# Kernel optimization log

Hardware: AMD Instinct MI355X
Metric: run time of the kernel (lower is better)

The kernel has to match this reference:

```python
import math
import jax, jax.numpy as jnp
import numpy as np

B, L, D, H = 4, 2048, 512, 8
DK = D // H  # d_keys = d_values = 64
KFAC = 3


def setup_inputs() -> dict:
    key = jax.random.key(0)
    ks = jax.random.split(key, 10)
    u_part = min(KFAC * int(math.ceil(math.log(L))), L)  # 24
    scale = 1.0 / math.sqrt(D)
    return {
        "queries": jax.random.normal(ks[0], (B, L, D), jnp.float32),
        "keys": jax.random.normal(ks[1], (B, L, D), jnp.float32),
        "values": jax.random.normal(ks[2], (B, L, D), jnp.float32),
        "index_sample": jax.random.randint(ks[3], (L, u_part), 0, L, jnp.int32),
        "Wq": jax.random.normal(ks[4], (D, D), jnp.float32) * scale,
        "bq": jnp.zeros((D,), jnp.float32),
        "Wk": jax.random.normal(ks[5], (D, D), jnp.float32) * scale,
        "bk": jnp.zeros((D,), jnp.float32),
        "Wv": jax.random.normal(ks[6], (D, D), jnp.float32) * scale,
        "bv": jnp.zeros((D,), jnp.float32),
        "Wo": jax.random.normal(ks[7], (D, D), jnp.float32) * scale,
        "bo": jnp.zeros((D,), jnp.float32),
    }


def reference(queries, keys, values, index_sample, Wq, bq, Wk, bk, Wv, bv, Wo, bo):
    b, q_len, d_out = queries.shape
    k_len = keys.shape[1]
    # projections -> [B, H, L, DK]
    q = (queries @ Wq + bq).reshape(b, q_len, H, DK).transpose(0, 2, 1, 3)
    k = (keys @ Wk + bk).reshape(b, k_len, H, DK).transpose(0, 2, 1, 3)
    v = (values @ Wv + bv).reshape(b, k_len, H, DK).transpose(0, 2, 1, 3)

    n_top = min(KFAC * int(math.ceil(math.log(q_len))), q_len)  # u

    # --- _prob_qk: sampled QK scores to pick sparse queries ---
    # k_sample: [B, H, q_len, sample_k, DK]
    k_sample = k[:, :, index_sample, :]
    q_k_sample = jnp.einsum("bhld,bhlsd->bhls", q, k_sample)
    m = jnp.max(q_k_sample, axis=-1) - jnp.sum(q_k_sample, axis=-1) / k_len
    _, m_top = jax.lax.top_k(m, n_top)  # [B, H, u]

    q_reduce = jnp.take_along_axis(q, m_top[..., None], axis=2)  # [B, H, u, DK]
    scores_top = jnp.einsum("bhud,bhkd->bhuk", q_reduce, k) / math.sqrt(d_out)

    # --- masked (causal) branch: mask_flag=True ---
    causal = jnp.triu(jnp.ones((q_len, k_len), bool), 1)
    indicator = causal[m_top]  # [B, H, u, k_len]
    scores_top = jnp.where(indicator, -jnp.inf, scores_top)

    attn = jax.nn.softmax(scores_top, axis=-1)  # [B, H, u, k_len]
    context = jnp.cumsum(v, axis=2)  # default context for non-selected queries
    attn_values = jnp.einsum("bhuk,bhkd->bhud", attn, v)

    bidx = jnp.arange(b)[:, None, None]
    hidx = jnp.arange(H)[None, :, None]
    context = context.at[bidx, hidx, m_top].set(attn_values)

    # mix=False: transpose back to [B, L, H, DV] then merge heads
    context = context.transpose(0, 2, 1, 3).reshape(b, q_len, H * DK)
    out = context @ Wo + bo  # dropout_rate=0 / inference: identity
    return out
```

## Files before the change

kernel.cpp:

```cpp
#include <hip/hip_runtime.h>
#include <hip/hip_bf16.h>
#include <math.h>

#define Bq 4
#define Lq 2048
#define Dq 512
#define Hq 8
#define DKq 64
#define Uq 24
#define TSCAN 16
#define NTILE (Lq / TSCAN)
#define NSUP 16
#define JCH 256
#define NCH (Lq / JCH)
#define TKCH 8

typedef unsigned short ushort_t;
typedef unsigned long long u64;
typedef __attribute__((ext_vector_type(8))) short bfrag8;
typedef __attribute__((ext_vector_type(4))) float facc4;

__device__ inline ushort_t bf16_rne(float f) {
  unsigned u = __float_as_uint(f);
  u += 0x7FFF + ((u >> 16) & 1);
  return (ushort_t)(u >> 16);
}
__device__ inline float bf16f(ushort_t h) {
  return __uint_as_float(((unsigned)h) << 16);
}
__device__ inline unsigned fkey(float f) {
  unsigned u = __float_as_uint(f);
  return (u & 0x80000000u) ? ~u : (u | 0x80000000u);
}
__device__ __forceinline__ void gl2lds16(const void* g, void* l) {
  __builtin_amdgcn_global_load_lds(
      (const __attribute__((address_space(1))) unsigned*)g,
      (__attribute__((address_space(3))) unsigned*)l, 16, 0, 0);
}

__global__ __launch_bounds__(256) void cast_all(
    const float* __restrict__ xq, const float* __restrict__ xk,
    const float* __restrict__ xv, ushort_t* __restrict__ qh,
    ushort_t* __restrict__ ql, ushort_t* __restrict__ kh,
    ushort_t* __restrict__ kl, ushort_t* __restrict__ vh) {
  int z = blockIdx.y;
  const float* x = z == 0 ? xq : (z == 1 ? xk : xv);
  ushort_t* hi = z == 0 ? qh : (z == 1 ? kh : vh);
  ushort_t* lo = z == 0 ? ql : kl;
  int t = blockIdx.x * 256 + threadIdx.x;
  float4 v = *(const float4*)&x[(size_t)t * 4];
  ushort_t h0 = bf16_rne(v.x), h1 = bf16_rne(v.y), h2 = bf16_rne(v.z),
           h3 = bf16_rne(v.w);
  ushort4 hh = {h0, h1, h2, h3};
  *(ushort4*)&hi[(size_t)t * 4] = hh;
  if (z < 2) {
    ushort4 ll = {bf16_rne(v.x - bf16f(h0)), bf16_rne(v.y - bf16f(h1)),
                  bf16_rne(v.z - bf16f(h2)), bf16_rne(v.w - bf16f(h3))};
    *(ushort4*)&lo[(size_t)t * 4] = ll;
  }
}

__global__ __launch_bounds__(256) void transpose_cast4(
    const float* __restrict__ W0, const float* __restrict__ W1,
    const float* __restrict__ W2, const float* __restrict__ W3,
    ushort_t* __restrict__ T0h, ushort_t* __restrict__ T0l,
    ushort_t* __restrict__ T1h, ushort_t* __restrict__ T1l,
    ushort_t* __restrict__ T2h, ushort_t* __restrict__ T3h) {
  __shared__ float tile[32][33];
  int z = blockIdx.z;
  const float* W = z == 0 ? W0 : (z == 1 ? W1 : (z == 2 ? W2 : W3));
  ushort_t* Th = z == 0 ? T0h : (z == 1 ? T1h : (z == 2 ? T2h : T3h));
  ushort_t* Tl = z == 0 ? T0l : (z == 1 ? T1l : nullptr);
  int k0 = blockIdx.x * 32, n0 = blockIdx.y * 32;
  int tx = threadIdx.x & 31, ty = threadIdx.x >> 5;
  for (int r = ty; r < 32; r += 8)
    tile[tx][r] = W[(size_t)(k0 + r) * 512 + n0 + tx];
  __syncthreads();
  for (int r = ty; r < 32; r += 8) {
    float v = tile[r][tx];
    ushort_t h = bf16_rne(v);
    Th[(size_t)(n0 + r) * 512 + k0 + tx] = h;
    if (Tl) Tl[(size_t)(n0 + r) * 512 + k0 + tx] = bf16_rne(v - bf16f(h));
  }
}

__global__ __launch_bounds__(256) void gemm_qkv(
    const ushort_t* __restrict__ Aqh, const ushort_t* __restrict__ Aql,
    const ushort_t* __restrict__ Akh, const ushort_t* __restrict__ Akl,
    const ushort_t* __restrict__ Avh,
    const ushort_t* __restrict__ Wqh, const ushort_t* __restrict__ Wql,
    const ushort_t* __restrict__ Wkh, const ushort_t* __restrict__ Wkl,
    const ushort_t* __restrict__ Wvh,
    const float* __restrict__ bq, const float* __restrict__ bk,
    const float* __restrict__ bv,
    float* __restrict__ qo, float* __restrict__ ko, float* __restrict__ vo) {
  __shared__ ushort_t Ash[128][32], Asl[128][32];
  __shared__ ushort_t Bsh[128][32], Bsl[128][32];
  int which = blockIdx.z;
  const ushort_t* Ah = which == 0 ? Aqh : (which == 1 ? Akh : Avh);
  const ushort_t* Al = which == 0 ? Aql : Akl;
  const ushort_t* Bh = which == 0 ? Wqh : (which == 1 ? Wkh : Wvh);
  const ushort_t* Bl = which == 0 ? Wql : Wkl;
  const float* bias = which == 0 ? bq : (which == 1 ? bk : bv);
  float* C = which == 0 ? qo : (which == 1 ? ko : vo);
  const bool split = which < 2;

  int bm = blockIdx.x, bn = blockIdx.y;
  int tid = threadIdx.x;
  int wave = tid >> 6, lane = tid & 63;
  int wm = (wave & 1) * 64, wn = (wave >> 1) * 64;
  int quad = lane >> 4, lm = lane & 15;
  int srow = tid >> 2;
  int slc = (((tid & 3) ^ ((tid >> 3) & 3))) * 8;
  int sphys = (tid & 3) * 8;
  int rsw = (quad ^ ((lm >> 1) & 3)) * 8;
  facc4 acc[4][4] = {};

  for (int k0 = 0; k0 < 512; k0 += 32) {
#pragma unroll
    for (int p = 0; p < 2; ++p) {
      int row = srow + p * 64;
      size_t ga = (size_t)(bm * 128 + row) * 512 + k0 + slc;
      size_t gb = (size_t)(bn * 128 + row) * 512 + k0 + slc;
      gl2lds16(&Ah[ga], &Ash[row][sphys]);
      gl2lds16(&Bh[gb], &Bsh[row][sphys]);
      if (split) {
        gl2lds16(&Al[ga], &Asl[row][sphys]);
        gl2lds16(&Bl[gb], &Bsl[row][sphys]);
      }
    }
    __syncthreads();
    bfrag8 afh[4], afl[4], bfh[4], bfl[4];
#pragma unroll
    for (int mt = 0; mt < 4; ++mt) {
      afh[mt] = *(bfrag8*)&Ash[wm + mt * 16 + lm][rsw];
      if (split) afl[mt] = *(bfrag8*)&Asl[wm + mt * 16 + lm][rsw];
    }
#pragma unroll
    for (int nt = 0; nt < 4; ++nt) {
      bfh[nt] = *(bfrag8*)&Bsh[wn + nt * 16 + lm][rsw];
      if (split) bfl[nt] = *(bfrag8*)&Bsl[wn + nt * 16 + lm][rsw];
    }
#pragma unroll
    for (int mt = 0; mt < 4; ++mt)
#pragma unroll
      for (int nt = 0; nt < 4; ++nt) {
        facc4 a = acc[mt][nt];
        a = __builtin_amdgcn_mfma_f32_16x16x32_bf16(afh[mt], bfh[nt], a, 0, 0, 0);
        if (split) {
          a = __builtin_amdgcn_mfma_f32_16x16x32_bf16(afl[mt], bfh[nt], a, 0, 0, 0);
          a = __builtin_amdgcn_mfma_f32_16x16x32_bf16(afh[mt], bfl[nt], a, 0, 0, 0);
        }
        acc[mt][nt] = a;
      }
    __syncthreads();
  }
#pragma unroll
  for (int mt = 0; mt < 4; ++mt)
#pragma unroll
    for (int nt = 0; nt < 4; ++nt) {
      int col = bn * 128 + wn + nt * 16 + lm;
      float bv2 = bias[col];
#pragma unroll
      for (int r = 0; r < 4; ++r) {
        int row = bm * 128 + wm + mt * 16 + quad * 4 + r;
        C[(size_t)row * 512 + col] = acc[mt][nt][r] + bv2;
      }
    }
}

__global__ __launch_bounds__(256) void gemm_bf16(
    const ushort_t* __restrict__ A, const ushort_t* __restrict__ Bt,
    const float* __restrict__ bias, float* __restrict__ C) {
  __shared__ ushort_t As[128][32];
  __shared__ ushort_t Bs[128][32];
  int bm = blockIdx.x, bn = blockIdx.y;
  int tid = threadIdx.x;
  int wave = tid >> 6, lane = tid & 63;
  int wm = (wave & 1) * 64, wn = (wave >> 1) * 64;
  int quad = lane >> 4, lm = lane & 15;
  int srow = tid >> 2;
  int slc = (((tid & 3) ^ ((tid >> 3) & 3))) * 8;
  int sphys = (tid & 3) * 8;
  int rsw = (quad ^ ((lm >> 1) & 3)) * 8;
  facc4 acc[4][4] = {};

  for (int k0 = 0; k0 < 512; k0 += 32) {
#pragma unroll
    for (int p = 0; p < 2; ++p) {
      int row = srow + p * 64;
      gl2lds16(&A[(size_t)(bm * 128 + row) * 512 + k0 + slc], &As[row][sphys]);
      gl2lds16(&Bt[(size_t)(bn * 128 + row) * 512 + k0 + slc], &Bs[row][sphys]);
    }
    __syncthreads();
    bfrag8 af[4], bf[4];
#pragma unroll
    for (int mt = 0; mt < 4; ++mt)
      af[mt] = *(bfrag8*)&As[wm + mt * 16 + lm][rsw];
#pragma unroll
    for (int nt = 0; nt < 4; ++nt)
      bf[nt] = *(bfrag8*)&Bs[wn + nt * 16 + lm][rsw];
#pragma unroll
    for (int mt = 0; mt < 4; ++mt)
#pragma unroll
      for (int nt = 0; nt < 4; ++nt)
        acc[mt][nt] = __builtin_amdgcn_mfma_f32_16x16x32_bf16(
            af[mt], bf[nt], acc[mt][nt], 0, 0, 0);
    __syncthreads();
  }
#pragma unroll
  for (int mt = 0; mt < 4; ++mt)
#pragma unroll
    for (int nt = 0; nt < 4; ++nt) {
      int col = bn * 128 + wn + nt * 16 + lm;
      float bv = bias[col];
#pragma unroll
      for (int r = 0; r < 4; ++r) {
        int row = bm * 128 + wm + mt * 16 + quad * 4 + r;
        C[(size_t)row * 512 + col] = acc[mt][nt][r] + bv;
      }
    }
}

__global__ __launch_bounds__(256) void compute_m(
    const float* __restrict__ q, const float* __restrict__ k,
    const int* __restrict__ idxs, float* __restrict__ m) {
  int wave = threadIdx.x >> 6, lane = threadIdx.x & 63;
  int lq = lane >> 4, dq = lane & 15;
  int slot = (blockIdx.x * 4 + wave) * 4 + lq;
  int l = slot & (Lq - 1);
  int bh = slot >> 11;
  int h = bh & (Hq - 1), b = bh >> 3;
  float4 qv = *(const float4*)&q[((size_t)b * Lq + l) * Dq + h * DKq + dq * 4];
  const float* kb = &k[(size_t)b * Lq * Dq + h * DKq + dq * 4];
  const int* ib = &idxs[l * Uq];
  float mx = -INFINITY, sm = 0.f;
#pragma unroll
  for (int s = 0; s < Uq; ++s) {
    int j = ib[s];
    float4 kv = *(const float4*)&kb[(size_t)j * Dq];
    float p = qv.x * kv.x + qv.y * kv.y + qv.z * kv.z + qv.w * kv.w;
    p += __shfl_xor(p, 1, 64);
    p += __shfl_xor(p, 2, 64);
    p += __shfl_xor(p, 4, 64);
    p += __shfl_xor(p, 8, 64);
    mx = fmaxf(mx, p);
    sm += p;
  }
  if (dq == 0) m[slot] = mx - sm * (1.0f / Lq);
}

__device__ inline void bitonic256_desc(u64* s, int tid) {
  for (int k = 2; k <= 256; k <<= 1) {
    for (int j = k >> 1; j > 0; j >>= 1) {
      int p = tid ^ j;
      u64 mine = s[tid], other = s[p];
      u64 mx = mine > other ? mine : other;
      u64 mn = mine > other ? other : mine;
      bool dir = (tid & k) == 0;
      bool lower = tid < p;
      u64 res = dir ? (lower ? mx : mn) : (lower ? mn : mx);
      __syncthreads();
      s[tid] = res;
      __syncthreads();
    }
  }
}

__global__ __launch_bounds__(256) void topk_stage1(
    const float* __restrict__ m, u64* __restrict__ cand) {
  __shared__ u64 s[256];
  int bh = blockIdx.x >> 3;
  int ch = blockIdx.x & 7;
  int tid = threadIdx.x;
  int gidx = ch * 256 + tid;
  float v = m[(size_t)bh * Lq + gidx];
  s[tid] = ((u64)fkey(v) << 32) | (u64)(Lq - 1 - gidx);
  __syncthreads();
  bitonic256_desc(s, tid);
  if (tid < Uq) cand[((size_t)bh * TKCH + ch) * Uq + tid] = s[tid];
}

__global__ __launch_bounds__(256) void topk_stage2(
    const u64* __restrict__ cand, int* __restrict__ mtop,
    int* __restrict__ repl) {
  __shared__ u64 s[256];
  __shared__ int mt[Uq];
  int bh = blockIdx.x;
  int tid = threadIdx.x;
  s[tid] = (tid < TKCH * Uq) ? cand[(size_t)bh * TKCH * Uq + tid] : 0ull;
  __syncthreads();
  bitonic256_desc(s, tid);
  if (tid < Uq) {
    int idx = Lq - 1 - (int)(s[tid] & 0xFFFFFFFFull);
    mtop[bh * Uq + tid] = idx;
    mt[tid] = idx;
  }
  __syncthreads();
  for (int l = tid; l < Lq; l += 256) {
    int u = -1;
#pragma unroll
    for (int t = 0; t < Uq; ++t)
      if (mt[t] == l) u = t;
    repl[(size_t)bh * Lq + l] = u;
  }
}

#define JT 256
#define JS 64

__global__ __launch_bounds__(256) void scores_kernel(
    const float* __restrict__ q, const float* __restrict__ k,
    const int* __restrict__ mtop, float* __restrict__ scg) {
  __shared__ float qs[Uq][DKq + 1];
  __shared__ float ks[JS][DKq + 1];
  __shared__ int i0s[Uq];
  int bh = blockIdx.y;
  int jt = blockIdx.x;
  int h = bh & (Hq - 1);
  int b = bh >> 3;
  int tid = threadIdx.x;
  if (tid < Uq) i0s[tid] = mtop[bh * Uq + tid];
  __syncthreads();
  for (int s = tid; s < Uq * 16; s += 256) {
    int u = s >> 4, qd = (s & 15) * 4;
    float4 t = *(const float4*)&q[((size_t)b * Lq + i0s[u]) * Dq + h * DKq + qd];
    qs[u][qd] = t.x; qs[u][qd + 1] = t.y; qs[u][qd + 2] = t.z; qs[u][qd + 3] = t.w;
  }
  int jp = tid & 31;
  int ug = tid >> 5;
  const float scale = 0.044194173824159216f;
  for (int sub = 0; sub < JT / JS; ++sub) {
    int jbase = jt * JT + sub * JS;
    __syncthreads();
    for (int s = tid; s < JS * 16; s += 256) {
      int j = s >> 4, qd = (s & 15) * 4;
      float4 t = *(const float4*)&k[((size_t)b * Lq + jbase + j) * Dq + h * DKq + qd];
      ks[j][qd] = t.x; ks[j][qd + 1] = t.y; ks[j][qd + 2] = t.z; ks[j][qd + 3] = t.w;
    }
    __syncthreads();
    float acc[3][2] = {};
    int j0 = jp * 2, j1 = j0 + 1;
#pragma unroll 8
    for (int d = 0; d < DKq; ++d) {
      float k0 = ks[j0][d], k1 = ks[j1][d];
#pragma unroll
      for (int uu = 0; uu < 3; ++uu) {
        float qv = qs[ug * 3 + uu][d];
        acc[uu][0] += qv * k0;
        acc[uu][1] += qv * k1;
      }
    }
#pragma unroll
    for (int uu = 0; uu < 3; ++uu) {
      int u = ug * 3 + uu;
      scg[((size_t)(bh * Uq + u)) * Lq + jbase + j0] = acc[uu][0] * scale;
      scg[((size_t)(bh * Uq + u)) * Lq + jbase + j1] = acc[uu][1] * scale;
    }
  }
}

__global__ __launch_bounds__(256) void softmax_pv_partial(
    const float* __restrict__ scg, const float* __restrict__ v,
    const int* __restrict__ mtop, float* __restrict__ pmax,
    float* __restrict__ psum, float* __restrict__ pvp) {
  int blk = blockIdx.y;
  int jc = blockIdx.x;
  int bh = blk / Uq;
  int h = bh & (Hq - 1);
  int b = bh >> 3;
  int n = mtop[blk] + 1;
  int j0 = jc * JCH;
  if (j0 >= n) return;
  int cnt = min(JCH, n - j0);
  int tid = threadIdx.x, wave = tid >> 6, lane = tid & 63;
  __shared__ float es[JCH];
  __shared__ float red[4][DKq];
  __shared__ float rr[4];

  const float* row = &scg[(size_t)blk * Lq + j0];
  float mx = (tid < cnt) ? row[tid] : -INFINITY;
#pragma unroll
  for (int off = 32; off; off >>= 1) mx = fmaxf(mx, __shfl_xor(mx, off, 64));
  if (lane == 0) rr[wave] = mx;
  __syncthreads();
  mx = fmaxf(fmaxf(rr[0], rr[1]), fmaxf(rr[2], rr[3]));
  __syncthreads();

  float e = (tid < cnt) ? __expf(row[tid] - mx) : 0.f;
  es[tid] = e;
  float sm = e;
#pragma unroll
  for (int off = 32; off; off >>= 1) sm += __shfl_xor(sm, off, 64);
  if (lane == 0) rr[wave] = sm;
  __syncthreads();

  float acc = 0.f;
  const float* vb = &v[((size_t)b * Lq + j0) * Dq + h * DKq + lane];
  int jlo = wave * 64;
  int jhi = min(jlo + 64, cnt);
#pragma unroll 4
  for (int j = jlo; j < jhi; ++j) acc += es[j] * vb[(size_t)j * Dq];
  red[wave][lane] = acc;
  __syncthreads();
  if (wave == 0) {
    if (lane == 0) {
      pmax[blk * NCH + jc] = mx;
      psum[blk * NCH + jc] = rr[0] + rr[1] + rr[2] + rr[3];
    }
    pvp[((size_t)blk * NCH + jc) * DKq + lane] =
        red[0][lane] + red[1][lane] + red[2][lane] + red[3][lane];
  }
}

__global__ __launch_bounds__(128) void tile_sum(const float* __restrict__ v,
                                                float* __restrict__ tsum) {
  int blk = blockIdx.x;
  int tile = blk & (NTILE - 1);
  int b = blk >> 7;
  int d4 = threadIdx.x;
  float4 s = {0.f, 0.f, 0.f, 0.f};
  const float* base = &v[((size_t)b * Lq + tile * TSCAN) * Dq + d4 * 4];
#pragma unroll
  for (int r = 0; r < TSCAN; ++r) {
    float4 x = *(const float4*)&base[(size_t)r * Dq];
    s.x += x.x; s.y += x.y; s.z += x.z; s.w += x.w;
  }
  *(float4*)&tsum[((size_t)b * NTILE + tile) * Dq + d4 * 4] = s;
}

__global__ __launch_bounds__(128) void stile_sum(
    const float* __restrict__ tsum, float* __restrict__ stsum) {
  int blk = blockIdx.x;
  int s = blk & (NSUP - 1);
  int b = blk >> 4;
  int d4 = threadIdx.x;
  float4 acc = {0.f, 0.f, 0.f, 0.f};
  const float* tb = &tsum[((size_t)b * NTILE + s * 8) * Dq + d4 * 4];
#pragma unroll
  for (int i = 0; i < 8; ++i) {
    float4 t = *(const float4*)&tb[(size_t)i * Dq];
    acc.x += t.x; acc.y += t.y; acc.z += t.z; acc.w += t.w;
  }
  *(float4*)&stsum[((size_t)b * NSUP + s) * Dq + d4 * 4] = acc;
}

__global__ __launch_bounds__(128) void build_context(
    const float* __restrict__ v, const float* __restrict__ tsum,
    const float* __restrict__ stsum, const int* __restrict__ repl,
    const float* __restrict__ pmax, const float* __restrict__ psum,
    const float* __restrict__ pvp, ushort_t* __restrict__ ctxh) {
  int blk = blockIdx.x;
  int tile = blk & (NTILE - 1);
  int b = blk >> 7;
  int d4 = threadIdx.x;
  int h = d4 >> 4;
  int sup = tile >> 3;
  float4 run = {0.f, 0.f, 0.f, 0.f};
  const float* sb = &stsum[(size_t)b * NSUP * Dq + d4 * 4];
  for (int s = 0; s < sup; ++s) {
    float4 t = *(const float4*)&sb[(size_t)s * Dq];
    run.x += t.x; run.y += t.y; run.z += t.z; run.w += t.w;
  }
  const float* tb = &tsum[((size_t)b * NTILE + sup * 8) * Dq + d4 * 4];
  int rem = tile & 7;
  for (int i = 0; i < rem; ++i) {
    float4 t = *(const float4*)&tb[(size_t)i * Dq];
    run.x += t.x; run.y += t.y; run.z += t.z; run.w += t.w;
  }
  const int* replb = &repl[(size_t)(b * Hq + h) * Lq + tile * TSCAN];
  const float* vb = &v[((size_t)b * Lq + tile * TSCAN) * Dq + d4 * 4];
  ushort_t* cb = &ctxh[((size_t)b * Lq + tile * TSCAN) * Dq + d4 * 4];
#pragma unroll
  for (int r = 0; r < TSCAN; ++r) {
    float4 x = *(const float4*)&vb[(size_t)r * Dq];
    run.x += x.x; run.y += x.y; run.z += x.z; run.w += x.w;
    int u = replb[r];
    float4 val = run;
    if (u >= 0) {
      int l = tile * TSCAN + r;
      int blku = (b * Hq + h) * Uq + u;
      int nc = (l + JCH) / JCH;
      float gmax = -INFINITY;
      for (int c = 0; c < nc; ++c) gmax = fmaxf(gmax, pmax[blku * NCH + c]);
      float tot = 0.f;
      float4 acc = {0.f, 0.f, 0.f, 0.f};
      for (int c = 0; c < nc; ++c) {
        float wgt = __expf(pmax[blku * NCH + c] - gmax);
        tot += psum[blku * NCH + c] * wgt;
        float4 pv = *(const float4*)&pvp[((size_t)blku * NCH + c) * DKq +
                                         (d4 & 15) * 4];
        acc.x += pv.x * wgt; acc.y += pv.y * wgt;
        acc.z += pv.z * wgt; acc.w += pv.w * wgt;
      }
      float inv = 1.0f / tot;
      val.x = acc.x * inv; val.y = acc.y * inv;
      val.z = acc.z * inv; val.w = acc.w * inv;
    }
    ushort4 o = {bf16_rne(val.x), bf16_rne(val.y), bf16_rne(val.z),
                 bf16_rne(val.w)};
    *(ushort4*)&cb[(size_t)r * Dq] = o;
  }
}

extern "C" void kernel_launch(void* const* d_in, const int* in_sizes, int n_in,
                              void* d_out, int out_size, void* d_ws,
                              size_t ws_size, hipStream_t stream) {
  const float* queries = (const float*)d_in[0];
  const float* keys    = (const float*)d_in[1];
  const float* values  = (const float*)d_in[2];
  const int*   idxs    = (const int*)d_in[3];
  const float* Wq = (const float*)d_in[4];
  const float* bq = (const float*)d_in[5];
  const float* Wk = (const float*)d_in[6];
  const float* bk = (const float*)d_in[7];
  const float* Wv = (const float*)d_in[8];
  const float* bv = (const float*)d_in[9];
  const float* Wo = (const float*)d_in[10];
  const float* bo = (const float*)d_in[11];
  float* out = (float*)d_out;

  const size_t BLD = (size_t)Bq * Lq * Dq;
  char* w = (char*)d_ws;
  float* q    = (float*)w; w += BLD * 4;
  float* k    = (float*)w; w += BLD * 4;
  float* v    = (float*)w; w += BLD * 4;
  float* scg  = (float*)w; w += (size_t)Bq * Hq * Uq * Lq * 4;
  float* m    = (float*)w; w += (size_t)Bq * Hq * Lq * 4;
  float* tsum = (float*)w; w += (size_t)Bq * NTILE * Dq * 4;
  float* stsum= (float*)w; w += (size_t)Bq * NSUP * Dq * 4;
  int* mtop   = (int*)w;   w += Bq * Hq * Uq * 4;
  int* repl   = (int*)w;   w += (size_t)Bq * Hq * Lq * 4;
  float* pmax = (float*)w; w += (size_t)Bq * Hq * Uq * NCH * 4;
  float* psum = (float*)w; w += (size_t)Bq * Hq * Uq * NCH * 4;
  float* pvp  = (float*)w; w += (size_t)Bq * Hq * Uq * NCH * DKq * 4;
  u64* cand   = (u64*)w;   w += (size_t)Bq * Hq * TKCH * Uq * 8;
  ushort_t* ctxh = (ushort_t*)w; w += BLD * 2;
  ushort_t* Aqh = (ushort_t*)w; w += BLD * 2;
  ushort_t* Aql = (ushort_t*)w; w += BLD * 2;
  ushort_t* Akh = (ushort_t*)w; w += BLD * 2;
  ushort_t* Akl = (ushort_t*)w; w += BLD * 2;
  ushort_t* Avh = (ushort_t*)w; w += BLD * 2;
  const size_t WSZ = 512 * 512;
  ushort_t* Wqh = (ushort_t*)w; w += WSZ * 2;
  ushort_t* Wql = (ushort_t*)w; w += WSZ * 2;
  ushort_t* Wkh = (ushort_t*)w; w += WSZ * 2;
  ushort_t* Wkl = (ushort_t*)w; w += WSZ * 2;
  ushort_t* Wvh = (ushort_t*)w; w += WSZ * 2;
  ushort_t* Woh = (ushort_t*)w; w += WSZ * 2;

  {
    dim3 tgrid(16, 16, 4);
    transpose_cast4<<<tgrid, 256, 0, stream>>>(Wq, Wk, Wv, Wo, Wqh, Wql, Wkh,
                                               Wkl, Wvh, Woh);
  }

  {
    dim3 cgrid(BLD / 4 / 256, 3);
    cast_all<<<cgrid, 256, 0, stream>>>(queries, keys, values, Aqh, Aql, Akh,
                                        Akl, Avh);
  }

  {
    dim3 ggrid(64, 4, 3);
    gemm_qkv<<<ggrid, 256, 0, stream>>>(Aqh, Aql, Akh, Akl, Avh, Wqh, Wql,
                                        Wkh, Wkl, Wvh, bq, bk, bv, q, k, v);
  }

  compute_m<<<(Bq * Hq * Lq) / 16, 256, 0, stream>>>(q, k, idxs, m);
  topk_stage1<<<Bq * Hq * TKCH, 256, 0, stream>>>(m, cand);
  topk_stage2<<<Bq * Hq, 256, 0, stream>>>(cand, mtop, repl);

  {
    dim3 sgrid(Lq / JT, Bq * Hq);
    scores_kernel<<<sgrid, 256, 0, stream>>>(q, k, mtop, scg);
  }
  {
    dim3 pgrid(NCH, Bq * Hq * Uq);
    softmax_pv_partial<<<pgrid, 256, 0, stream>>>(scg, v, mtop, pmax, psum, pvp);
  }

  tile_sum<<<Bq * NTILE, 128, 0, stream>>>(v, tsum);
  stile_sum<<<Bq * NSUP, 128, 0, stream>>>(tsum, stsum);
  build_context<<<Bq * NTILE, 128, 0, stream>>>(v, tsum, stsum, repl, pmax,
                                                psum, pvp, ctxh);

  {
    dim3 ggrid(64, 4);
    gemm_bf16<<<ggrid, 256, 0, stream>>>(ctxh, Woh, bo, out);
  }
}
```

Baseline: 275.9 us.

## Merge prep kernels, fuse two-stage top-k, drop super-tile prefix kernel

Folds the weight transpose-cast into the activation cast kernel as one launch, with the extra grid row handling weights. Replaces the two bitonic-sort top-k kernels with a single per-head kernel that runs 24 rounds of register argmax plus a wave-shuffle reduction, and writes the replacement map directly. Removes the super-tile sum kernel, so build_context scans up to 127 tile sums serially. This saves three launches and the candidate buffer, at the cost of a longer serial prefix loop in build_context and a top-k that runs on only 32 blocks.

```diff
diff --git a/kernel.cpp b/kernel.cpp
--- a/kernel.cpp
+++ b/kernel.cpp
@@ -10,7 +10,6 @@
 #define Uq 24
 #define TSCAN 16
 #define NTILE (Lq / TSCAN)
-#define NSUP 16
 #define JCH 256
 #define NCH (Lq / JCH)
 #define TKCH 8
@@ -38,40 +37,42 @@
       (__attribute__((address_space(3))) unsigned*)l, 16, 0, 0);
 }
 
-__global__ __launch_bounds__(256) void cast_all(
+__global__ __launch_bounds__(256) void prep_all(
     const float* __restrict__ xq, const float* __restrict__ xk,
     const float* __restrict__ xv, ushort_t* __restrict__ qh,
     ushort_t* __restrict__ ql, ushort_t* __restrict__ kh,
-    ushort_t* __restrict__ kl, ushort_t* __restrict__ vh) {
-  int z = blockIdx.y;
-  const float* x = z == 0 ? xq : (z == 1 ? xk : xv);
-  ushort_t* hi = z == 0 ? qh : (z == 1 ? kh : vh);
-  ushort_t* lo = z == 0 ? ql : kl;
-  int t = blockIdx.x * 256 + threadIdx.x;
-  float4 v = *(const float4*)&x[(size_t)t * 4];
-  ushort_t h0 = bf16_rne(v.x), h1 = bf16_rne(v.y), h2 = bf16_rne(v.z),
-           h3 = bf16_rne(v.w);
-  ushort4 hh = {h0, h1, h2, h3};
-  *(ushort4*)&hi[(size_t)t * 4] = hh;
-  if (z < 2) {
-    ushort4 ll = {bf16_rne(v.x - bf16f(h0)), bf16_rne(v.y - bf16f(h1)),
-                  bf16_rne(v.z - bf16f(h2)), bf16_rne(v.w - bf16f(h3))};
-    *(ushort4*)&lo[(size_t)t * 4] = ll;
-  }
-}
-
-__global__ __launch_bounds__(256) void transpose_cast4(
+    ushort_t* __restrict__ kl, ushort_t* __restrict__ vh,
     const float* __restrict__ W0, const float* __restrict__ W1,
     const float* __restrict__ W2, const float* __restrict__ W3,
     ushort_t* __restrict__ T0h, ushort_t* __restrict__ T0l,
     ushort_t* __restrict__ T1h, ushort_t* __restrict__ T1l,
     ushort_t* __restrict__ T2h, ushort_t* __restrict__ T3h) {
   __shared__ float tile[32][33];
-  int z = blockIdx.z;
+  int y = blockIdx.y;
+  if (y < 3) {
+    const float* x = y == 0 ? xq : (y == 1 ? xk : xv);
+    ushort_t* hi = y == 0 ? qh : (y == 1 ? kh : vh);
+    ushort_t* lo = y == 0 ? ql : kl;
+    int t = blockIdx.x * 256 + threadIdx.x;
+    float4 v = *(const float4*)&x[(size_t)t * 4];
+    ushort_t h0 = bf16_rne(v.x), h1 = bf16_rne(v.y), h2 = bf16_rne(v.z),
+             h3 = bf16_rne(v.w);
+    ushort4 hh = {h0, h1, h2, h3};
+    *(ushort4*)&hi[(size_t)t * 4] = hh;
+    if (y < 2) {
+      ushort4 ll = {bf16_rne(v.x - bf16f(h0)), bf16_rne(v.y - bf16f(h1)),
+                    bf16_rne(v.z - bf16f(h2)), bf16_rne(v.w - bf16f(h3))};
+      *(ushort4*)&lo[(size_t)t * 4] = ll;
+    }
+    return;
+  }
+  int id = blockIdx.x;
+  if (id >= 1024) return;
+  int z = id >> 8;
   const float* W = z == 0 ? W0 : (z == 1 ? W1 : (z == 2 ? W2 : W3));
   ushort_t* Th = z == 0 ? T0h : (z == 1 ? T1h : (z == 2 ? T2h : T3h));
   ushort_t* Tl = z == 0 ? T0l : (z == 1 ? T1l : nullptr);
-  int k0 = blockIdx.x * 32, n0 = blockIdx.y * 32;
+  int k0 = ((id >> 4) & 15) * 32, n0 = (id & 15) * 32;
   int tx = threadIdx.x & 31, ty = threadIdx.x >> 5;
   for (int r = ty; r < 32; r += 8)
     tile[tx][r] = W[(size_t)(k0 + r) * 512 + n0 + tx];
@@ -250,60 +251,51 @@
   if (dq == 0) m[slot] = mx - sm * (1.0f / Lq);
 }
 
-__device__ inline void bitonic256_desc(u64* s, int tid) {
-  for (int k = 2; k <= 256; k <<= 1) {
-    for (int j = k >> 1; j > 0; j >>= 1) {
-      int p = tid ^ j;
-      u64 mine = s[tid], other = s[p];
-      u64 mx = mine > other ? mine : other;
-      u64 mn = mine > other ? other : mine;
-      bool dir = (tid & k) == 0;
-      bool lower = tid < p;
-      u64 res = dir ? (lower ? mx : mn) : (lower ? mn : mx);
-      __syncthreads();
-      s[tid] = res;
-      __syncthreads();
-    }
-  }
-}
-
-__global__ __launch_bounds__(256) void topk_stage1(
-    const float* __restrict__ m, u64* __restrict__ cand) {
-  __shared__ u64 s[256];
-  int bh = blockIdx.x >> 3;
-  int ch = blockIdx.x & 7;
-  int tid = threadIdx.x;
-  int gidx = ch * 256 + tid;
-  float v = m[(size_t)bh * Lq + gidx];
-  s[tid] = ((u64)fkey(v) << 32) | (u64)(Lq - 1 - gidx);
-  __syncthreads();
-  bitonic256_desc(s, tid);
-  if (tid < Uq) cand[((size_t)bh * TKCH + ch) * Uq + tid] = s[tid];
-}
-
-__global__ __launch_bounds__(256) void topk_stage2(
-    const u64* __restrict__ cand, int* __restrict__ mtop,
+__global__ __launch_bounds__(256) void topk_fused(
+    const float* __restrict__ m, int* __restrict__ mtop,
     int* __restrict__ repl) {
-  __shared__ u64 s[256];
+  __shared__ u64 red[2][4];
   __shared__ int mt[Uq];
   int bh = blockIdx.x;
-  int tid = threadIdx.x;
-  s[tid] = (tid < TKCH * Uq) ? cand[(size_t)bh * TKCH * Uq + tid] : 0ull;
-  __syncthreads();
-  bitonic256_desc(s, tid);
-  if (tid < Uq) {
-    int idx = Lq - 1 - (int)(s[tid] & 0xFFFFFFFFull);
-    mtop[bh * Uq + tid] = idx;
-    mt[tid] = idx;
-  }
-  __syncthreads();
-  for (int l = tid; l < Lq; l += 256) {
-    int u = -1;
-#pragma unroll
-    for (int t = 0; t < Uq; ++t)
-      if (mt[t] == l) u = t;
-    repl[(size_t)bh * Lq + l] = u;
-  }
+  int tid = threadIdx.x, wave = tid >> 6, lane = tid & 63;
+  u64 keys[TKCH];
+#pragma unroll
+  for (int c = 0; c < TKCH; ++c) {
+    int gidx = c * 256 + tid;
+    float v = m[(size_t)bh * Lq + gidx];
+    keys[c] = ((u64)fkey(v) << 32) | (u64)(Lq - 1 - gidx);
+  }
+#pragma unroll 1
+  for (int it = 0; it < Uq; ++it) {
+    u64 lb = keys[0];
+#pragma unroll
+    for (int c = 1; c < TKCH; ++c) lb = keys[c] > lb ? keys[c] : lb;
+#pragma unroll
+    for (int off = 32; off; off >>= 1) {
+      u64 o = __shfl_xor(lb, off, 64);
+      lb = o > lb ? o : lb;
+    }
+    int p = it & 1;
+    if (lane == 0) red[p][wave] = lb;
+    __syncthreads();
+    u64 w0 = red[p][0] > red[p][1] ? red[p][0] : red[p][1];
+    u64 w1 = red[p][2] > red[p][3] ? red[p][2] : red[p][3];
+    u64 win = w0 > w1 ? w0 : w1;
+    if (tid == 0) {
+      int idx = Lq - 1 - (int)(win & 0xFFFFFFFFull);
+      mtop[bh * Uq + it] = idx;
+      mt[it] = idx;
+    }
+#pragma unroll
+    for (int c = 0; c < TKCH; ++c)
+      if (keys[c] == win) keys[c] = 0;
+  }
+  __syncthreads();
+  int* rb = &repl[(size_t)bh * Lq];
+#pragma unroll
+  for (int c = 0; c < TKCH; ++c) rb[c * 256 + tid] = -1;
+  __syncthreads();
+  if (tid < Uq) rb[mt[tid]] = tid;
 }
 
 #define JT 256
@@ -429,25 +421,9 @@
   *(float4*)&tsum[((size_t)b * NTILE + tile) * Dq + d4 * 4] = s;
 }
 
-__global__ __launch_bounds__(128) void stile_sum(
-    const float* __restrict__ tsum, float* __restrict__ stsum) {
-  int blk = blockIdx.x;
-  int s = blk & (NSUP - 1);
-  int b = blk >> 4;
-  int d4 = threadIdx.x;
-  float4 acc = {0.f, 0.f, 0.f, 0.f};
-  const float* tb = &tsum[((size_t)b * NTILE + s * 8) * Dq + d4 * 4];
-#pragma unroll
-  for (int i = 0; i < 8; ++i) {
-    float4 t = *(const float4*)&tb[(size_t)i * Dq];
-    acc.x += t.x; acc.y += t.y; acc.z += t.z; acc.w += t.w;
-  }
-  *(float4*)&stsum[((size_t)b * NSUP + s) * Dq + d4 * 4] = acc;
-}
-
 __global__ __launch_bounds__(128) void build_context(
     const float* __restrict__ v, const float* __restrict__ tsum,
-    const float* __restrict__ stsum, const int* __restrict__ repl,
+    const int* __restrict__ repl,
     const float* __restrict__ pmax, const float* __restrict__ psum,
     const float* __restrict__ pvp, ushort_t* __restrict__ ctxh) {
   int blk = blockIdx.x;
@@ -455,18 +431,12 @@
   int b = blk >> 7;
   int d4 = threadIdx.x;
   int h = d4 >> 4;
-  int sup = tile >> 3;
   float4 run = {0.f, 0.f, 0.f, 0.f};
-  const float* sb = &stsum[(size_t)b * NSUP * Dq + d4 * 4];
-  for (int s = 0; s < sup; ++s) {
-    float4 t = *(const float4*)&sb[(size_t)s * Dq];
-    run.x += t.x; run.y += t.y; run.z += t.z; run.w += t.w;
-  }
-  const float* tb = &tsum[((size_t)b * NTILE + sup * 8) * Dq + d4 * 4];
-  int rem = tile & 7;
-  for (int i = 0; i < rem; ++i) {
-    float4 t = *(const float4*)&tb[(size_t)i * Dq];
-    run.x += t.x; run.y += t.y; run.z += t.z; run.w += t.w;
+  const float* tb = &tsum[(size_t)b * NTILE * Dq + d4 * 4];
+#pragma unroll 4
+  for (int t = 0; t < tile; ++t) {
+    float4 x = *(const float4*)&tb[(size_t)t * Dq];
+    run.x += x.x; run.y += x.y; run.z += x.z; run.w += x.w;
   }
   const int* replb = &repl[(size_t)(b * Hq + h) * Lq + tile * TSCAN];
   const float* vb = &v[((size_t)b * Lq + tile * TSCAN) * Dq + d4 * 4];
@@ -528,13 +498,11 @@
   float* scg  = (float*)w; w += (size_t)Bq * Hq * Uq * Lq * 4;
   float* m    = (float*)w; w += (size_t)Bq * Hq * Lq * 4;
   float* tsum = (float*)w; w += (size_t)Bq * NTILE * Dq * 4;
-  float* stsum= (float*)w; w += (size_t)Bq * NSUP * Dq * 4;
   int* mtop   = (int*)w;   w += Bq * Hq * Uq * 4;
   int* repl   = (int*)w;   w += (size_t)Bq * Hq * Lq * 4;
   float* pmax = (float*)w; w += (size_t)Bq * Hq * Uq * NCH * 4;
   float* psum = (float*)w; w += (size_t)Bq * Hq * Uq * NCH * 4;
   float* pvp  = (float*)w; w += (size_t)Bq * Hq * Uq * NCH * DKq * 4;
-  u64* cand   = (u64*)w;   w += (size_t)Bq * Hq * TKCH * Uq * 8;
   ushort_t* ctxh = (ushort_t*)w; w += BLD * 2;
   ushort_t* Aqh = (ushort_t*)w; w += BLD * 2;
   ushort_t* Aql = (ushort_t*)w; w += BLD * 2;
@@ -550,15 +518,10 @@
   ushort_t* Woh = (ushort_t*)w; w += WSZ * 2;
 
   {
-    dim3 tgrid(16, 16, 4);
-    transpose_cast4<<<tgrid, 256, 0, stream>>>(Wq, Wk, Wv, Wo, Wqh, Wql, Wkh,
-                                               Wkl, Wvh, Woh);
-  }
-
-  {
-    dim3 cgrid(BLD / 4 / 256, 3);
-    cast_all<<<cgrid, 256, 0, stream>>>(queries, keys, values, Aqh, Aql, Akh,
-                                        Akl, Avh);
+    dim3 pgrid(BLD / 4 / 256, 4);
+    prep_all<<<pgrid, 256, 0, stream>>>(queries, keys, values, Aqh, Aql, Akh,
+                                        Akl, Avh, Wq, Wk, Wv, Wo, Wqh, Wql,
+                                        Wkh, Wkl, Wvh, Woh);
   }
 
   {
@@ -568,8 +531,7 @@
   }
 
   compute_m<<<(Bq * Hq * Lq) / 16, 256, 0, stream>>>(q, k, idxs, m);
-  topk_stage1<<<Bq * Hq * TKCH, 256, 0, stream>>>(m, cand);
-  topk_stage2<<<Bq * Hq, 256, 0, stream>>>(cand, mtop, repl);
+  topk_fused<<<Bq * Hq, 256, 0, stream>>>(m, mtop, repl);
 
   {
     dim3 sgrid(Lq / JT, Bq * Hq);
@@ -581,9 +543,8 @@
   }
 
   tile_sum<<<Bq * NTILE, 128, 0, stream>>>(v, tsum);
-  stile_sum<<<Bq * NSUP, 128, 0, stream>>>(tsum, stsum);
-  build_context<<<Bq * NTILE, 128, 0, stream>>>(v, tsum, stsum, repl, pmax,
-                                                psum, pvp, ctxh);
+  build_context<<<Bq * NTILE, 128, 0, stream>>>(v, tsum, repl, pmax, psum,
+                                                pvp, ctxh);
 
   {
     dim3 ggrid(64, 4);
```

After: 279.1 us. No clear change (+1.2%).
